# Optimization experiments

Hardware: AMD Instinct MI355X
Metric: run time of the kernel (lower is better)

Reference implementation:

```python
import jax, jax.numpy as jnp
import numpy as np

B, T, D, H = 4, 2048, 768, 12
DH = D // H
SCALE = DH ** 0.5


def setup_inputs() -> dict:
    key = jax.random.key(0)
    k1, k2, k3, k4, k5, k6 = jax.random.split(key, 6)
    h = jax.random.normal(k1, (B, T, D), dtype=jnp.float32)
    key_padding_mask = jax.random.bernoulli(k2, 0.1, (B, T))
    s = 1.0 / np.sqrt(D)
    Wq = jax.random.normal(k3, (D, D), dtype=jnp.float32) * s
    Wk = jax.random.normal(k4, (D, D), dtype=jnp.float32) * s
    Wv = jax.random.normal(k5, (D, D), dtype=jnp.float32) * s
    Wo = jax.random.normal(k6, (D, D), dtype=jnp.float32) * s
    return {"h": h, "key_padding_mask": key_padding_mask,
            "Wq": Wq, "Wk": Wk, "Wv": Wv, "Wo": Wo}


def _split_heads(x):
    Bb, Tt, _ = x.shape
    return x.reshape(Bb, Tt, H, DH).transpose(0, 2, 1, 3)  # [B,H,T,Dh]


def reference(h, key_padding_mask, Wq, Wk, Wv, Wo):
    # torch nn.Linear (no bias): y = x @ W.T
    Q = _split_heads(h @ Wq.T)
    K = _split_heads(h @ Wk.T)
    V = _split_heads(h @ Wv.T)
    scores = jnp.einsum('bhqd,bhkd->bhqk', Q, K) / SCALE
    k_pad = key_padding_mask[:, None, None, :]  # mask padded keys
    q_pad = key_padding_mask[:, None, :, None]  # padded query rows
    scores = jnp.where(k_pad, jnp.float32(-1e9), scores)
    scores = jnp.where(q_pad, jnp.float32(0.0), scores)
    attn = jax.nn.softmax(scores, axis=-1)  # stable softmax (same math)
    attn = jnp.where(q_pad, jnp.float32(0.0), attn)
    out = jnp.einsum('bhqk,bhkd->bhqd', attn, V)  # [B,H,T,Dh]
    out = out.transpose(0, 2, 1, 3).reshape(B, T, D)
    return out @ Wo.T
```

## Files before the change

### kernel.cpp

```cpp
#include <hip/hip_runtime.h>
#include <stdint.h>

typedef __bf16 bf16x8 __attribute__((ext_vector_type(8)));
typedef float  f32x4  __attribute__((ext_vector_type(4)));
typedef unsigned short u16x4 __attribute__((ext_vector_type(4)));

#define MFMA16(a,b,c) __builtin_amdgcn_mfma_f32_16x16x32_bf16((a),(b),(c),0,0,0)

constexpr int Bc  = 4;
constexpr int Tc  = 2048;
constexpr int Dc  = 768;
constexpr int Hc  = 12;
constexpr int NTOK = Bc * Tc;
constexpr int QKV_LD = 3 * Dc;

static __device__ __forceinline__ unsigned short f2bf(float f){
  unsigned u = __float_as_uint(f);
  u += 0x7fffu + ((u >> 16) & 1u);
  return (unsigned short)(u >> 16);
}

static __device__ __forceinline__ float exp2a(float x){
  float r; asm("v_exp_f32 %0, %1" : "=v"(r) : "v"(x)); return r;
}

static __device__ __forceinline__ float max3f(float a, float b, float c){
  float r; asm("v_max3_f32 %0, %1, %2, %3" : "=v"(r) : "v"(a), "v"(b), "v"(c)); return r;
}

static __device__ __forceinline__ unsigned cvtpk_bf16(float lo, float hi){
  unsigned r; asm("v_cvt_pk_bf16_f32 %0, %1, %2" : "=v"(r) : "v"(lo), "v"(hi)); return r;
}

static __device__ __forceinline__ void gload_lds16(const void* g, void* l){
  __builtin_amdgcn_global_load_lds((__attribute__((address_space(1))) void*)g,
                                   (__attribute__((address_space(3))) void*)l,
                                   16, 0, 0);
}

__global__ void cvt_bf16(const float* __restrict__ src, unsigned short* __restrict__ dst,
                         int n4, float scale){
  int i = blockIdx.x * blockDim.x + threadIdx.x;
  if (i >= n4) return;
  float4 v = reinterpret_cast<const float4*>(src)[i];
  ushort4 o;
  o.x = f2bf(v.x * scale); o.y = f2bf(v.y * scale);
  o.z = f2bf(v.z * scale); o.w = f2bf(v.w * scale);
  reinterpret_cast<ushort4*>(dst)[i] = o;
}

__global__ void expand_mask(const unsigned* __restrict__ raw, int* __restrict__ out, int n){
  __shared__ int sInt, sFlt;
  int t = threadIdx.x;
  if (t == 0){ sInt = 1; sFlt = 1; }
  __syncthreads();
  int okI = 1, okF = 1;
  for (int i = t; i < n/4; i += blockDim.x){
    unsigned u = raw[i];
    okI &= (u <= 1u);
    okF &= (u == 0u || u == 0x3f800000u);
  }
  if (!okI) atomicAnd(&sInt, 0);
  if (!okF) atomicAnd(&sFlt, 0);
  __syncthreads();
  if (sInt || sFlt){
    for (int i = t; i < n; i += blockDim.x) out[i] = (raw[i] != 0u);
  } else {
    const unsigned char* rb = (const unsigned char*)raw;
    for (int i = t; i < n; i += blockDim.x) out[i] = (rb[i] != 0);
  }
}

template<typename CT>
__global__ __launch_bounds__(256) void gemm_bt(const unsigned short* __restrict__ A,
                                               const unsigned short* __restrict__ Bm,
                                               CT* __restrict__ C,
                                               int M, int N, int K){
  __shared__ unsigned short As[128*32];
  __shared__ unsigned short Bs[128*32];
  const int t = threadIdx.x;
  const int w = t >> 6, l = t & 63;
  const int wr = w >> 1, wc = w & 1;
  const int br = blockIdx.y * 128, bc = blockIdx.x * 128;

  f32x4 acc[4][4];
  const f32x4 fz = {0.f,0.f,0.f,0.f};
  #pragma unroll
  for (int m=0;m<4;m++)
    #pragma unroll
    for (int n=0;n<4;n++) acc[m][n] = fz;

  const int lrow = l >> 2;
  const int lk   = (l & 3) * 8;
  const int fr   = l & 15;
  const int fk   = (l >> 4) * 8;

  for (int k0 = 0; k0 < K; k0 += 32){
    #pragma unroll
    for (int it = 0; it < 2; ++it){
      const int rb = it*64 + w*16;
      gload_lds16(A  + (size_t)(br + rb + lrow)*K + k0 + lk, &As[rb*32]);
      gload_lds16(Bm + (size_t)(bc + rb + lrow)*K + k0 + lk, &Bs[rb*32]);
    }
    __syncthreads();
    bf16x8 a[4], b[4];
    #pragma unroll
    for (int m=0;m<4;m++)
      a[m] = *reinterpret_cast<const bf16x8*>(&As[(wr*64 + m*16 + fr)*32 + fk]);
    #pragma unroll
    for (int n=0;n<4;n++)
      b[n] = *reinterpret_cast<const bf16x8*>(&Bs[(wc*64 + n*16 + fr)*32 + fk]);
    #pragma unroll
    for (int m=0;m<4;m++)
      #pragma unroll
      for (int n=0;n<4;n++)
        acc[m][n] = MFMA16(a[m], b[n], acc[m][n]);
    __syncthreads();
  }

  const int orow0 = br + wr*64 + (l >> 4)*4;
  const int ocol0 = bc + wc*64 + (l & 15);
  #pragma unroll
  for (int m=0;m<4;m++)
    #pragma unroll
    for (int n=0;n<4;n++)
      #pragma unroll
      for (int r=0;r<4;r++){
        const size_t idx = (size_t)(orow0 + m*16 + r) * N + (ocol0 + n*16);
        float v = acc[m][n][r];
        if constexpr (sizeof(CT) == 2) C[idx] = (CT)f2bf(v);
        else                           C[idx] = v;
      }
}

__global__ __launch_bounds__(256) void vtrans(const unsigned short* __restrict__ QKV,
                                              unsigned short* __restrict__ VtG){
  __shared__ unsigned short st[64][72];
  const int t = threadIdx.x;
  const int token0 = blockIdx.x * 64;
  const int bh = blockIdx.y;
  const int b = bh / Hc, h = bh - b * Hc;
  const size_t tokbase = (size_t)b * Tc;

  const int tok = t >> 2;
  const unsigned short* src = QKV + (tokbase + token0 + tok) * (size_t)QKV_LD + 1536 + h*64;
  #pragma unroll
  for (int i = 0; i < 2; ++i){
    const int ul = (t & 3)*2 + i;
    *reinterpret_cast<uint4*>(&st[tok][ul*8]) =
        *reinterpret_cast<const uint4*>(src + ul*8);
  }
  __syncthreads();
  const int d = t >> 2;
  #pragma unroll
  for (int half = 0; half < 2; ++half){
    union { unsigned short s[8]; uint4 q; } tmp;
    const int tk0 = (t & 3)*8 + half*32;
    #pragma unroll
    for (int j = 0; j < 8; ++j)
      tmp.s[j] = st[tk0 + j][d];
    *reinterpret_cast<uint4*>(VtG + ((size_t)(bh*64 + d))*Tc + token0 + tk0) = tmp.q;
  }
}

__global__ __launch_bounds__(256, 4) void attn(const unsigned short* __restrict__ QKV,
                                               const unsigned short* __restrict__ VtG,
                                               const int* __restrict__ mask,
                                               unsigned short* __restrict__ AO){
  __shared__ unsigned short Ks[2][64*64];
  __shared__ unsigned short Vs[2][64*64];
  __shared__ float Ms[2][64];

  const int t = threadIdx.x, w = t >> 6, l = t & 63;
  const int bh = blockIdx.y;
  const int b  = bh / Hc, h = bh - b * Hc;
  const int q0 = blockIdx.x * 128 + w * 32;
  const int fr = l & 15, fg = l >> 4;

  const size_t tokbase = (size_t)b * Tc;
  const unsigned short* Qp = QKV + (tokbase + q0) * (size_t)QKV_LD + h*64;
  const unsigned short* Kbase = QKV + tokbase * (size_t)QKV_LD + h*64 + 768;
  const unsigned short* VtB = VtG + (size_t)(bh*64) * Tc;
  const int* bm = mask + b * Tc;

  bf16x8 qa[2][2];
  #pragma unroll
  for (int mc=0; mc<2; mc++)
    #pragma unroll
    for (int ks=0; ks<2; ks++)
      qa[mc][ks] = *reinterpret_cast<const bf16x8*>(
          Qp + (size_t)(mc*16+fr)*QKV_LD + ks*32 + fg*8);

  unsigned bits = 0;
  if (w == 0){
    #pragma unroll
    for (int cc = 0; cc < 32; ++cc)
      bits |= (unsigned)(bm[cc*64 + l] != 0) << cc;
  }

  const f32x4 fz = {0.f,0.f,0.f,0.f};
  f32x4 accT[2][4];
  #pragma unroll
  for (int mc=0; mc<2; mc++)
    #pragma unroll
    for (int n=0; n<4; n++) accT[mc][n] = fz;
  float mrow[2] = {-1e30f, -1e30f};
  float lsum[2] = {0.f, 0.f};

  const int srow = l >> 3, scol = (l & 7) ^ (l >> 3);
  auto stage = [&](int c){
    const int key0 = c * 64, buf = c & 1;
    #pragma unroll
    for (int i=0; i<2; i++){
      const int rb = w*16 + i*8;
      gload_lds16(Kbase + (size_t)(key0 + rb + srow)*QKV_LD + scol*8,
                  &Ks[buf][rb*64]);
    }
    #pragma unroll
    for (int i=0; i<2; i++){
      const int rb = (w*2 + i)*8;
      gload_lds16(VtB + (size_t)(rb + srow)*Tc + key0 + scol*8,
                  &Vs[buf][rb*64]);
    }
  };

  stage(0);
  if (w == 0) Ms[0][l] = (bits & 1u) ? -1e9f : 0.f;
  asm volatile("s_waitcnt vmcnt(0) lgkmcnt(0)" ::: "memory");
  __builtin_amdgcn_s_barrier();
  asm volatile("" ::: "memory");

  #pragma unroll 2
  for (int c = 0; c < 32; ++c){
    const int cb = c & 1;

    f32x4 S[2][4];
    __builtin_amdgcn_s_setprio(1);
    #pragma unroll
    for (int g=0; g<4; g++){
      f32x4 mb = *reinterpret_cast<const f32x4*>(&Ms[cb][g*16 + fg*4]);
      S[0][g] = mb; S[1][g] = mb;
      #pragma unroll
      for (int ks=0; ks<2; ks++){
        const int row = g*16 + fr;
        bf16x8 kf = *reinterpret_cast<const bf16x8*>(
            &Ks[cb][row*64 + (((ks*4+fg) ^ (row&7))*8)]);
        S[0][g] = MFMA16(kf, qa[0][ks], S[0][g]);
        S[1][g] = MFMA16(kf, qa[1][ks], S[1][g]);
      }
    }
    __builtin_amdgcn_s_setprio(0);

    if (c + 1 < 32) stage(c + 1);

    unsigned pkAll[2][4][2];
    #pragma unroll
    for (int mc=0; mc<2; mc++){
      float a0 = max3f(S[mc][0][0], S[mc][0][1], S[mc][0][2]);
      float a1 = max3f(S[mc][0][3], S[mc][1][0], S[mc][1][1]);
      float a2 = max3f(S[mc][1][2], S[mc][1][3], S[mc][2][0]);
      float a3 = max3f(S[mc][2][1], S[mc][2][2], S[mc][2][3]);
      float a4 = max3f(S[mc][3][0], S[mc][3][1], S[mc][3][2]);
      float cm = fmaxf(max3f(a0, a1, a2), max3f(a3, a4, S[mc][3][3]));
      cm = fmaxf(cm, __shfl_xor(cm, 16));
      cm = fmaxf(cm, __shfl_xor(cm, 32));
      if (!__all(cm <= mrow[mc] + 8.0f)){
        const float nm = fmaxf(mrow[mc], cm);
        const float sc = exp2a(mrow[mc] - nm);
        lsum[mc] *= sc;
        #pragma unroll
        for (int n=0; n<4; n++) accT[mc][n] = accT[mc][n] * sc;
        mrow[mc] = nm;
      }
      float ps = 0.f;
      #pragma unroll
      for (int g=0; g<4; g++){
        const float p0 = exp2a(S[mc][g][0] - mrow[mc]);
        const float p1 = exp2a(S[mc][g][1] - mrow[mc]);
        const float p2 = exp2a(S[mc][g][2] - mrow[mc]);
        const float p3 = exp2a(S[mc][g][3] - mrow[mc]);
        ps += (p0 + p1) + (p2 + p3);
        pkAll[mc][g][0] = cvtpk_bf16(p0, p1);
        pkAll[mc][g][1] = cvtpk_bf16(p2, p3);
      }
      ps += __shfl_xor(ps, 16);
      ps += __shfl_xor(ps, 32);
      lsum[mc] += ps;
    }

    __builtin_amdgcn_s_setprio(1);
    #pragma unroll
    for (int ks2=0; ks2<2; ks2++){
      union PBu { unsigned u[4]; bf16x8 v; } pb0, pb1;
      pb0.u[0] = pkAll[0][ks2*2][0];   pb0.u[1] = pkAll[0][ks2*2][1];
      pb0.u[2] = pkAll[0][ks2*2+1][0]; pb0.u[3] = pkAll[0][ks2*2+1][1];
      pb1.u[0] = pkAll[1][ks2*2][0];   pb1.u[1] = pkAll[1][ks2*2][1];
      pb1.u[2] = pkAll[1][ks2*2+1][0]; pb1.u[3] = pkAll[1][ks2*2+1][1];
      #pragma unroll
      for (int n=0; n<4; n++){
        const int row = n*16 + fr;
        union VA { u16x4 h[2]; bf16x8 v; } va;
        va.h[0] = *reinterpret_cast<const u16x4*>(
            &Vs[cb][row*64 + (((ks2*4     + (fg>>1)) ^ (row&7))*8) + (fg&1)*4]);
        va.h[1] = *reinterpret_cast<const u16x4*>(
            &Vs[cb][row*64 + (((ks2*4 + 2 + (fg>>1)) ^ (row&7))*8) + (fg&1)*4]);
        accT[0][n] = MFMA16(va.v, pb0.v, accT[0][n]);
        accT[1][n] = MFMA16(va.v, pb1.v, accT[1][n]);
      }
    }
    __builtin_amdgcn_s_setprio(0);

    if (w == 0 && c + 1 < 32)
      Ms[cb^1][l] = ((bits >> (c+1)) & 1u) ? -1e9f : 0.f;

    if (c < 31){
      asm volatile("s_waitcnt vmcnt(0) lgkmcnt(0)" ::: "memory");
      __builtin_amdgcn_s_barrier();
      asm volatile("" ::: "memory");
    }
  }

  #pragma unroll
  for (int mc=0; mc<2; mc++){
    const int qrow = q0 + mc*16 + fr;
    const int qm = bm[qrow];
    const float inv = (qm || lsum[mc] <= 0.f) ? 0.f : 1.f / lsum[mc];
    #pragma unroll
    for (int n=0; n<4; n++){
      ushort4 o;
      o.x = f2bf(accT[mc][n][0] * inv);
      o.y = f2bf(accT[mc][n][1] * inv);
      o.z = f2bf(accT[mc][n][2] * inv);
      o.w = f2bf(accT[mc][n][3] * inv);
      *reinterpret_cast<ushort4*>(
          &AO[(tokbase + qrow) * (size_t)Dc + h*64 + n*16 + fg*4]) = o;
    }
  }
}

extern "C" void kernel_launch(void* const* d_in, const int* in_sizes, int n_in,
                              void* d_out, int out_size, void* d_ws, size_t ws_size,
                              hipStream_t stream){
  const float* h    = (const float*)d_in[0];
  const unsigned* m = (const unsigned*)d_in[1];
  const float* Wq   = (const float*)d_in[2];
  const float* Wk   = (const float*)d_in[3];
  const float* Wv   = (const float*)d_in[4];
  const float* Wo   = (const float*)d_in[5];
  float* out        = (float*)d_out;

  unsigned short* hb   = (unsigned short*)d_ws;
  unsigned short* Wqkv = hb   + (size_t)NTOK * Dc;
  unsigned short* Wob  = Wqkv + (size_t)QKV_LD * Dc;
  unsigned short* QKV  = Wob  + (size_t)Dc * Dc;
  unsigned short* AO   = QKV  + (size_t)NTOK * QKV_LD;
  int* mexp            = (int*)(AO + (size_t)NTOK * Dc);

  const size_t need = ((size_t)NTOK*Dc + (size_t)QKV_LD*Dc + (size_t)Dc*Dc +
                       (size_t)NTOK*QKV_LD + (size_t)NTOK*Dc) * 2 + (size_t)NTOK*4;
  if (ws_size < need) return;

  const int W2 = Dc * Dc;
  cvt_bf16<<<(NTOK*Dc/4 + 255)/256, 256, 0, stream>>>(h,  hb,          NTOK*Dc/4, 1.0f);
  cvt_bf16<<<(W2/4 + 255)/256,      256, 0, stream>>>(Wq, Wqkv,        W2/4, 0.125f*1.44269504f);
  cvt_bf16<<<(W2/4 + 255)/256,      256, 0, stream>>>(Wk, Wqkv + W2,   W2/4, 1.0f);
  cvt_bf16<<<(W2/4 + 255)/256,      256, 0, stream>>>(Wv, Wqkv + 2*W2, W2/4, 1.0f);
  cvt_bf16<<<(W2/4 + 255)/256,      256, 0, stream>>>(Wo, Wob,         W2/4, 1.0f);
  expand_mask<<<1, 256, 0, stream>>>(m, mexp, NTOK);

  gemm_bt<unsigned short><<<dim3(QKV_LD/128, NTOK/128), 256, 0, stream>>>(
      hb, Wqkv, QKV, NTOK, QKV_LD, Dc);

  unsigned short* VtG = hb;
  vtrans<<<dim3(Tc/64, Bc*Hc), 256, 0, stream>>>(QKV, VtG);

  attn<<<dim3(Tc/128, Bc*Hc), 256, 0, stream>>>(QKV, VtG, mexp, AO);

  gemm_bt<float><<<dim3(Dc/128, NTOK/128), 256, 0, stream>>>(
      AO, Wob, out, NTOK, Dc, Dc);
}
```

Baseline: 192.2 us.

## Halve attention query tile per block and swizzle block-to-head mapping

```diff
diff --git a/kernel.cpp b/kernel.cpp
--- a/kernel.cpp
+++ b/kernel.cpp
@@ -172,9 +172,12 @@
   __shared__ float Ms[2][64];
 
   const int t = threadIdx.x, w = t >> 6, l = t & 63;
-  const int bh = blockIdx.y;
+  const int lin = blockIdx.y * gridDim.x + blockIdx.x;
+  const int swz = (lin & 7) * 192 + (lin >> 3);
+  const int qt  = swz & 31;
+  const int bh  = swz >> 5;
   const int b  = bh / Hc, h = bh - b * Hc;
-  const int q0 = blockIdx.x * 128 + w * 32;
+  const int q0 = qt * 64 + w * 16;
   const int fr = l & 15, fg = l >> 4;
 
   const size_t tokbase = (size_t)b * Tc;
@@ -183,13 +186,11 @@
   const unsigned short* VtB = VtG + (size_t)(bh*64) * Tc;
   const int* bm = mask + b * Tc;
 
-  bf16x8 qa[2][2];
-  #pragma unroll
-  for (int mc=0; mc<2; mc++)
-    #pragma unroll
-    for (int ks=0; ks<2; ks++)
-      qa[mc][ks] = *reinterpret_cast<const bf16x8*>(
-          Qp + (size_t)(mc*16+fr)*QKV_LD + ks*32 + fg*8);
+  bf16x8 qa[2];
+  #pragma unroll
+  for (int ks=0; ks<2; ks++)
+    qa[ks] = *reinterpret_cast<const bf16x8*>(
+        Qp + (size_t)fr*QKV_LD + ks*32 + fg*8);
 
   unsigned bits = 0;
   if (w == 0){
@@ -199,13 +200,10 @@
   }
 
   const f32x4 fz = {0.f,0.f,0.f,0.f};
-  f32x4 accT[2][4];
-  #pragma unroll
-  for (int mc=0; mc<2; mc++)
-    #pragma unroll
-    for (int n=0; n<4; n++) accT[mc][n] = fz;
-  float mrow[2] = {-1e30f, -1e30f};
-  float lsum[2] = {0.f, 0.f};
+  f32x4 accT[4];
+  #pragma unroll
+  for (int n=0; n<4; n++) accT[n] = fz;
+  float mrow = -1e30f, lsum = 0.f;
 
   const int srow = l >> 3, scol = (l & 7) ^ (l >> 3);
   auto stage = [&](int c){
@@ -234,68 +232,63 @@
   for (int c = 0; c < 32; ++c){
     const int cb = c & 1;
 
-    f32x4 S[2][4];
+    f32x4 S[4];
     __builtin_amdgcn_s_setprio(1);
     #pragma unroll
     for (int g=0; g<4; g++){
-      f32x4 mb = *reinterpret_cast<const f32x4*>(&Ms[cb][g*16 + fg*4]);
-      S[0][g] = mb; S[1][g] = mb;
+      S[g] = *reinterpret_cast<const f32x4*>(&Ms[cb][g*16 + fg*4]);
       #pragma unroll
       for (int ks=0; ks<2; ks++){
         const int row = g*16 + fr;
         bf16x8 kf = *reinterpret_cast<const bf16x8*>(
             &Ks[cb][row*64 + (((ks*4+fg) ^ (row&7))*8)]);
-        S[0][g] = MFMA16(kf, qa[0][ks], S[0][g]);
-        S[1][g] = MFMA16(kf, qa[1][ks], S[1][g]);
+        S[g] = MFMA16(kf, qa[ks], S[g]);
       }
     }
     __builtin_amdgcn_s_setprio(0);
 
     if (c + 1 < 32) stage(c + 1);
 
-    unsigned pkAll[2][4][2];
-    #pragma unroll
-    for (int mc=0; mc<2; mc++){
-      float a0 = max3f(S[mc][0][0], S[mc][0][1], S[mc][0][2]);
-      float a1 = max3f(S[mc][0][3], S[mc][1][0], S[mc][1][1]);
-      float a2 = max3f(S[mc][1][2], S[mc][1][3], S[mc][2][0]);
-      float a3 = max3f(S[mc][2][1], S[mc][2][2], S[mc][2][3]);
-      float a4 = max3f(S[mc][3][0], S[mc][3][1], S[mc][3][2]);
-      float cm = fmaxf(max3f(a0, a1, a2), max3f(a3, a4, S[mc][3][3]));
+    unsigned pkAll[4][2];
+    {
+      float a0 = max3f(S[0][0], S[0][1], S[0][2]);
+      float a1 = max3f(S[0][3], S[1][0], S[1][1]);
+      float a2 = max3f(S[1][2], S[1][3], S[2][0]);
+      float a3 = max3f(S[2][1], S[2][2], S[2][3]);
+      float a4 = max3f(S[3][0], S[3][1], S[3][2]);
+      float cm = fmaxf(max3f(a0, a1, a2), max3f(a3, a4, S[3][3]));
       cm = fmaxf(cm, __shfl_xor(cm, 16));
       cm = fmaxf(cm, __shfl_xor(cm, 32));
-      if (!__all(cm <= mrow[mc] + 8.0f)){
-        const float nm = fmaxf(mrow[mc], cm);
-        const float sc = exp2a(mrow[mc] - nm);
-        lsum[mc] *= sc;
+      if (!__all(cm <= mrow + 8.0f)){
+        const float nm = fmaxf(mrow, cm);
+        const float sc = exp2a(mrow - nm);
+        lsum *= sc;
         #pragma unroll
-        for (int n=0; n<4; n++) accT[mc][n] = accT[mc][n] * sc;
-        mrow[mc] = nm;
+        for (int n=0; n<4; n++) accT[n] = accT[n] * sc;
+        mrow = nm;
       }
       float ps = 0.f;
       #pragma unroll
       for (int g=0; g<4; g++){
-        const float p0 = exp2a(S[mc][g][0] - mrow[mc]);
-        const float p1 = exp2a(S[mc][g][1] - mrow[mc]);
-        const float p2 = exp2a(S[mc][g][2] - mrow[mc]);
-        const float p3 = exp2a(S[mc][g][3] - mrow[mc]);
+        const float p0 = exp2a(S[g][0] - mrow);
+        const float p1 = exp2a(S[g][1] - mrow);
+        const float p2 = exp2a(S[g][2] - mrow);
+        const float p3 = exp2a(S[g][3] - mrow);
         ps += (p0 + p1) + (p2 + p3);
-        pkAll[mc][g][0] = cvtpk_bf16(p0, p1);
-        pkAll[mc][g][1] = cvtpk_bf16(p2, p3);
+        pkAll[g][0] = cvtpk_bf16(p0, p1);
+        pkAll[g][1] = cvtpk_bf16(p2, p3);
       }
       ps += __shfl_xor(ps, 16);
       ps += __shfl_xor(ps, 32);
-      lsum[mc] += ps;
+      lsum += ps;
     }
 
     __builtin_amdgcn_s_setprio(1);
     #pragma unroll
     for (int ks2=0; ks2<2; ks2++){
-      union PBu { unsigned u[4]; bf16x8 v; } pb0, pb1;
-      pb0.u[0] = pkAll[0][ks2*2][0];   pb0.u[1] = pkAll[0][ks2*2][1];
-      pb0.u[2] = pkAll[0][ks2*2+1][0]; pb0.u[3] = pkAll[0][ks2*2+1][1];
-      pb1.u[0] = pkAll[1][ks2*2][0];   pb1.u[1] = pkAll[1][ks2*2][1];
-      pb1.u[2] = pkAll[1][ks2*2+1][0]; pb1.u[3] = pkAll[1][ks2*2+1][1];
+      union PBu { unsigned u[4]; bf16x8 v; } pb;
+      pb.u[0] = pkAll[ks2*2][0];   pb.u[1] = pkAll[ks2*2][1];
+      pb.u[2] = pkAll[ks2*2+1][0]; pb.u[3] = pkAll[ks2*2+1][1];
       #pragma unroll
       for (int n=0; n<4; n++){
         const int row = n*16 + fr;
@@ -304,8 +297,7 @@
             &Vs[cb][row*64 + (((ks2*4     + (fg>>1)) ^ (row&7))*8) + (fg&1)*4]);
         va.h[1] = *reinterpret_cast<const u16x4*>(
             &Vs[cb][row*64 + (((ks2*4 + 2 + (fg>>1)) ^ (row&7))*8) + (fg&1)*4]);
-        accT[0][n] = MFMA16(va.v, pb0.v, accT[0][n]);
-        accT[1][n] = MFMA16(va.v, pb1.v, accT[1][n]);
+        accT[n] = MFMA16(va.v, pb.v, accT[n]);
       }
     }
     __builtin_amdgcn_s_setprio(0);
@@ -320,18 +312,17 @@
     }
   }
 
-  #pragma unroll
-  for (int mc=0; mc<2; mc++){
-    const int qrow = q0 + mc*16 + fr;
+  {
+    const int qrow = q0 + fr;
     const int qm = bm[qrow];
-    const float inv = (qm || lsum[mc] <= 0.f) ? 0.f : 1.f / lsum[mc];
+    const float inv = (qm || lsum <= 0.f) ? 0.f : 1.f / lsum;
     #pragma unroll
     for (int n=0; n<4; n++){
       ushort4 o;
-      o.x = f2bf(accT[mc][n][0] * inv);
-      o.y = f2bf(accT[mc][n][1] * inv);
-      o.z = f2bf(accT[mc][n][2] * inv);
-      o.w = f2bf(accT[mc][n][3] * inv);
+      o.x = f2bf(accT[n][0] * inv);
+      o.y = f2bf(accT[n][1] * inv);
+      o.z = f2bf(accT[n][2] * inv);
+      o.w = f2bf(accT[n][3] * inv);
       *reinterpret_cast<ushort4*>(
           &AO[(tokbase + qrow) * (size_t)Dc + h*64 + n*16 + fg*4]) = o;
     }
@@ -374,7 +365,7 @@
   unsigned short* VtG = hb;
   vtrans<<<dim3(Tc/64, Bc*Hc), 256, 0, stream>>>(QKV, VtG);
 
-  attn<<<dim3(Tc/128, Bc*Hc), 256, 0, stream>>>(QKV, VtG, mexp, AO);
+  attn<<<dim3(32, Bc*Hc), 256, 0, stream>>>(QKV, VtG, mexp, AO);
 
   gemm_bt<float><<<dim3(Dc/128, NTOK/128), 256, 0, stream>>>(
       AO, Wob, out, NTOK, Dc, Dc);
```

After: 210.9 us. 9.8% more time.
